# Performance work log

Hardware: AMD Instinct MI355X
Metric: run time of the kernel (lower is better)

## Reference

```python
import jax, jax.numpy as jnp
import numpy as np

B, N, M, H, NH = 128, 4096, 64, 512, 4
IN, OUT = 256, 256
NH2 = 2 * NH  # read/write heads interleaved: even idx = read, odd idx = write
EPS = 1e-8


def setup_inputs() -> dict:
    key = jax.random.key(0)
    ks = jax.random.split(key, 20)
    nrm = lambda k, shape, s=0.05: (jax.random.normal(k, shape, jnp.float32) * s)
    return {
        'in_data': jax.random.normal(ks[0], (B, IN), jnp.float32),
        'memory': jax.random.normal(ks[1], (B, N, M), jnp.float32) * 0.1,
        'h_prev': jax.random.normal(ks[2], (B, H), jnp.float32),
        'c_prev': jax.random.normal(ks[3], (B, H), jnp.float32),
        'prev_reads': jax.random.normal(ks[4], (NH, B, M), jnp.float32),
        'prev_weights': jax.random.uniform(ks[5], (NH2, B, N), jnp.float32),
        # controller LSTMCell (input = in_data ++ prev_reads)
        'W_ih': nrm(ks[6], (4 * H, IN + NH * M)),
        'b_ih': jnp.zeros((4 * H,), jnp.float32),
        'W_hh': nrm(ks[7], (4 * H, H)),
        'b_hh': jnp.zeros((4 * H,), jnp.float32),
        # output layer over [h ++ reads]
        'W_out': nrm(ks[8], (OUT, H + NH * M)),
        'b_out': jnp.zeros((OUT,), jnp.float32),
        # per-head addressing params, stacked over the 2*NH heads (fed with c-state)
        'Wk': nrm(ks[9], (NH2, M, H)), 'bk': jnp.zeros((NH2, M), jnp.float32),
        'Wbeta': nrm(ks[10], (NH2, H)), 'bbeta': jnp.zeros((NH2,), jnp.float32),
        'Wg': nrm(ks[11], (NH2, H)), 'bg': jnp.zeros((NH2,), jnp.float32),
        'Ws': nrm(ks[12], (NH2, 3, H)), 'bs': jnp.zeros((NH2, 3), jnp.float32),
        'Wgam': nrm(ks[13], (NH2, H)), 'bgam': jnp.zeros((NH2,), jnp.float32),
        'We': nrm(ks[14], (NH2, M, H)), 'be': jnp.zeros((NH2, M), jnp.float32),
        'Wa': nrm(ks[15], (NH2, M, H)), 'ba': jnp.zeros((NH2, M), jnp.float32),
    }


def reference(in_data, memory, h_prev, c_prev, prev_reads, prev_weights,
              W_ih, b_ih, W_hh, b_hh, W_out, b_out,
              Wk, bk, Wbeta, bbeta, Wg, bg, Ws, bs, Wgam, bgam, We, be, Wa, ba):
    bsz = in_data.shape[0]
    # controller LSTM step on [x ++ prev_reads]
    x = jnp.concatenate([in_data, jnp.swapaxes(prev_reads, 0, 1).reshape(bsz, -1)], axis=-1)
    gates = x @ W_ih.T + h_prev @ W_hh.T + b_ih + b_hh
    gi, gf, gg, go = jnp.split(gates, 4, axis=-1)
    c = jax.nn.sigmoid(gf) * c_prev + jax.nn.sigmoid(gi) * jnp.tanh(gg)
    h = jax.nn.sigmoid(go) * jnp.tanh(c)  # |h| < 1, so clamp(-20, 20) is identity

    mem = memory
    reads = []
    for i in range(NH2):  # fixed small loop; even = read head, odd = write head
        keyv = c @ Wk[i].T + bk[i]                                    # [B, M]
        beta = jax.nn.softplus(c @ Wbeta[i] + bbeta[i])[:, None]      # [B, 1]
        g = jax.nn.sigmoid(c @ Wg[i] + bg[i])[:, None]                # [B, 1]
        s = jax.nn.softmax(c @ Ws[i].T + bs[i], axis=-1)              # [B, 3]
        gamma = 1.0 + jax.nn.softplus(c @ Wgam[i] + bgam[i])[:, None]  # [B, 1]
        # content addressing: cosine similarity, sharpened softmax
        sim = jnp.einsum('bnm,bm->bn', mem, keyv)
        sim = sim / (jnp.linalg.norm(mem, axis=-1) * jnp.linalg.norm(keyv, axis=-1, keepdims=True) + EPS)
        wc = jax.nn.softmax(beta * sim, axis=-1)
        # interpolate, circular shift (-1, 0, +1), sharpen
        wg_ = g * wc + (1.0 - g) * prev_weights[i]
        wsft = (s[:, 0:1] * jnp.roll(wg_, -1, axis=1)
                + s[:, 1:2] * wg_
                + s[:, 2:3] * jnp.roll(wg_, 1, axis=1))
        wpow = wsft ** gamma
        w = wpow / (jnp.sum(wpow, axis=1, keepdims=True) + EPS)
        if i % 2 == 0:
            reads.append(jnp.einsum('bn,bnm->bm', w, mem))
        else:
            e = jax.nn.sigmoid(c @ We[i].T + be[i])                   # erase [B, M]
            a = jnp.tanh(c @ Wa[i].T + ba[i])                         # add   [B, M]
            mem = mem * (1.0 - w[:, :, None] * e[:, None, :]) + w[:, :, None] * a[:, None, :]

    out = jax.nn.sigmoid(jnp.concatenate([h] + reads, axis=-1) @ W_out.T + b_out)
    return out
```

## Files before the change

### kernel.cpp

```cpp
#include <hip/hip_runtime.h>
#include <math.h>

#define BSZ 128
#define NN_ 4096
#define MM_ 64
#define HH_ 512
#define EPSF 1e-8f

__device__ __forceinline__ float sigmoidf_(float x) { return 1.0f / (1.0f + expf(-x)); }
__device__ __forceinline__ float softplusf_(float x) { return fmaxf(x, 0.0f) + log1pf(expf(-fabsf(x))); }

__global__ void k_build_x(const float* __restrict__ in_data, const float* __restrict__ prev_reads,
                          float* __restrict__ x) {
    int idx = blockIdx.x * blockDim.x + threadIdx.x;
    if (idx >= BSZ * 512) return;
    int b = idx >> 9, j = idx & 511;
    float v;
    if (j < 256) v = in_data[b * 256 + j];
    else {
        int hi = (j - 256) >> 6, m = (j - 256) & 63;
        v = prev_reads[(hi * BSZ + b) * 64 + m];
    }
    x[idx] = v;
}

__global__ __launch_bounds__(256) void k_gemm_atk(const float* __restrict__ A,
                                                  const float* __restrict__ W,
                                                  float* __restrict__ C, int Ncols, int K) {
    __shared__ float Alds[64 * 129];
    __shared__ float Wlds[64 * 65];
    int t = threadIdx.x;
    int k0 = blockIdx.y * 64;
    int n0 = blockIdx.x * 64;
    for (int i = 0; i < 8; ++i) {
        int f = t + 256 * i;
        int row = f >> 4, kk = (f & 15) * 4;
        float4 v = *(const float4*)(A + (size_t)row * K + k0 + kk);
        Alds[(kk + 0) * 129 + row] = v.x;
        Alds[(kk + 1) * 129 + row] = v.y;
        Alds[(kk + 2) * 129 + row] = v.z;
        Alds[(kk + 3) * 129 + row] = v.w;
    }
    for (int i = 0; i < 4; ++i) {
        int f = t + 256 * i;
        int o = f >> 4, kk = (f & 15) * 4;
        float4 v = *(const float4*)(W + (size_t)(n0 + o) * K + k0 + kk);
        Wlds[(kk + 0) * 65 + o] = v.x;
        Wlds[(kk + 1) * 65 + o] = v.y;
        Wlds[(kk + 2) * 65 + o] = v.z;
        Wlds[(kk + 3) * 65 + o] = v.w;
    }
    __syncthreads();
    int ob = (t & 15) * 4;
    int bb = (t >> 4) * 8;
    float acc[4][8];
#pragma unroll
    for (int i = 0; i < 4; ++i)
#pragma unroll
        for (int j = 0; j < 8; ++j) acc[i][j] = 0.f;
    for (int kk = 0; kk < 64; ++kk) {
        const float* wp = &Wlds[kk * 65 + ob];
        const float* ap = &Alds[kk * 129 + bb];
        float w0 = wp[0], w1 = wp[1], w2 = wp[2], w3 = wp[3];
#pragma unroll
        for (int j = 0; j < 8; ++j) {
            float av = ap[j];
            acc[0][j] = fmaf(w0, av, acc[0][j]);
            acc[1][j] = fmaf(w1, av, acc[1][j]);
            acc[2][j] = fmaf(w2, av, acc[2][j]);
            acc[3][j] = fmaf(w3, av, acc[3][j]);
        }
    }
#pragma unroll
    for (int i = 0; i < 4; ++i)
#pragma unroll
        for (int j = 0; j < 8; ++j)
            atomicAdd(&C[(size_t)(bb + j) * Ncols + n0 + ob + i], acc[i][j]);
}

__global__ void k_lstm(const float* __restrict__ gates, const float* __restrict__ b_ih,
                       const float* __restrict__ b_hh, const float* __restrict__ c_prev,
                       float* __restrict__ cbuf, float* __restrict__ hbuf) {
    int idx = blockIdx.x * blockDim.x + threadIdx.x;
    if (idx >= BSZ * HH_) return;
    int b = idx >> 9, j = idx & 511;
    const float* gr = gates + (size_t)b * 2048;
    float gi = gr[j]        + b_ih[j]        + b_hh[j];
    float gf = gr[512 + j]  + b_ih[512 + j]  + b_hh[512 + j];
    float gg = gr[1024 + j] + b_ih[1024 + j] + b_hh[1024 + j];
    float go = gr[1536 + j] + b_ih[1536 + j] + b_hh[1536 + j];
    float cc = sigmoidf_(gf) * c_prev[idx] + sigmoidf_(gi) * tanhf(gg);
    float hh = sigmoidf_(go) * tanhf(cc);
    cbuf[idx] = cc;
    hbuf[idx] = hh;
}

__global__ void k_build_whead(const float* __restrict__ Wk, const float* __restrict__ bk,
                              const float* __restrict__ Wbeta, const float* __restrict__ bbeta,
                              const float* __restrict__ Wg, const float* __restrict__ bg,
                              const float* __restrict__ Ws, const float* __restrict__ bs,
                              const float* __restrict__ Wgam, const float* __restrict__ bgam,
                              const float* __restrict__ We, const float* __restrict__ be,
                              const float* __restrict__ Wa, const float* __restrict__ ba,
                              float* __restrict__ Whead, float* __restrict__ bhead) {
    int idx = blockIdx.x * blockDim.x + threadIdx.x;
    if (idx >= 1600 * 512) return;
    int r = idx >> 9, k = idx & 511;
    float v = 0.f, bv = 0.f;
    if (r < 1584) {
        int i = r / 198, q = r - i * 198;
        if (q < 64)       { v = Wk[((i << 6) + q) * 512 + k];        bv = bk[(i << 6) + q]; }
        else if (q == 64) { v = Wbeta[i * 512 + k];                  bv = bbeta[i]; }
        else if (q == 65) { v = Wg[i * 512 + k];                     bv = bg[i]; }
        else if (q <= 68) { v = Ws[(i * 3 + q - 66) * 512 + k];      bv = bs[i * 3 + q - 66]; }
        else if (q == 69) { v = Wgam[i * 512 + k];                   bv = bgam[i]; }
        else if (q < 134) { v = We[((i << 6) + q - 70) * 512 + k];   bv = be[(i << 6) + q - 70]; }
        else              { v = Wa[((i << 6) + q - 134) * 512 + k];  bv = ba[(i << 6) + q - 134]; }
    }
    Whead[idx] = v;
    if (k == 0) bhead[r] = bv;
}

__global__ __launch_bounds__(256) void k_headact(const float* __restrict__ Chead, const float* __restrict__ bhead,
                                                 float* __restrict__ keys, float* __restrict__ knorm,
                                                 float* __restrict__ betaA, float* __restrict__ gA,
                                                 float* __restrict__ gammaA, float* __restrict__ sA,
                                                 float* __restrict__ eA, float* __restrict__ aA) {
    __shared__ float sk[64];
    __shared__ float s3[3];
    int blk = blockIdx.x;
    int i = blk >> 7, b = blk & 127;
    int q = threadIdx.x;
    float val = 0.f;
    if (q < 198) val = Chead[(size_t)b * 1600 + i * 198 + q] + bhead[i * 198 + q];
    if (q < 64) { keys[(size_t)(i * BSZ + b) * 64 + q] = val; sk[q] = val * val; }
    if (q >= 66 && q <= 68) s3[q - 66] = val;
    __syncthreads();
    if (q == 0) {
        float s = 0.f;
        for (int m2 = 0; m2 < 64; ++m2) s += sk[m2];
        knorm[i * BSZ + b] = sqrtf(s);
    }
    if (q == 64) betaA[i * BSZ + b] = softplusf_(val);
    if (q == 65) gA[i * BSZ + b] = sigmoidf_(val);
    if (q == 69) gammaA[i * BSZ + b] = 1.f + softplusf_(val);
    if (q == 66) {
        float mx = fmaxf(s3[0], fmaxf(s3[1], s3[2]));
        float e0 = expf(s3[0] - mx), e1 = expf(s3[1] - mx), e2 = expf(s3[2] - mx);
        float inv = 1.f / (e0 + e1 + e2);
        sA[(i * BSZ + b) * 3 + 0] = e0 * inv;
        sA[(i * BSZ + b) * 3 + 1] = e1 * inv;
        sA[(i * BSZ + b) * 3 + 2] = e2 * inv;
    }
    if (q >= 70 && q < 134)  eA[(size_t)(i * BSZ + b) * 64 + (q - 70)] = sigmoidf_(val);
    if (q >= 134 && q < 198) aA[(size_t)(i * BSZ + b) * 64 + (q - 134)] = tanhf(val);
}

__global__ __launch_bounds__(256) void k_pass(float* __restrict__ mem,
                                              const float* __restrict__ w_read,
                                              const float* __restrict__ w_write,
                                              const float* __restrict__ e_w, const float* __restrict__ a_w,
                                              const float* __restrict__ k0, const float* __restrict__ k1,
                                              const float* __restrict__ kn0, const float* __restrict__ kn1,
                                              float* __restrict__ sim0, float* __restrict__ sim1,
                                              float* __restrict__ r_out,
                                              int has_read, int has_write, int nsims) {
    __shared__ __align__(16) float rbuf[16][64];
    int t = threadIdx.x;
    int lane = t & 15, grp = t >> 4;
    int base = blockIdx.x * 64;
    int b = base >> 12;
    int m4 = lane * 4;
    float4 e4 = make_float4(0.f, 0.f, 0.f, 0.f), a4 = e4, k0v = e4, k1v = e4;
    float kn0v = 0.f, kn1v = 0.f;
    if (has_write) {
        e4 = *(const float4*)(e_w + b * 64 + m4);
        a4 = *(const float4*)(a_w + b * 64 + m4);
    }
    if (nsims > 0) { k0v = *(const float4*)(k0 + b * 64 + m4); kn0v = kn0[b]; }
    if (nsims > 1) { k1v = *(const float4*)(k1 + b * 64 + m4); kn1v = kn1[b]; }
    float4 racc = make_float4(0.f, 0.f, 0.f, 0.f);
    for (int it = 0; it < 4; ++it) {
        int row = base + it * 16 + grp;
        float4 v = *(const float4*)(mem + (size_t)row * 64 + m4);
        if (has_read) {
            float wr = w_read[row];
            racc.x = fmaf(wr, v.x, racc.x);
            racc.y = fmaf(wr, v.y, racc.y);
            racc.z = fmaf(wr, v.z, racc.z);
            racc.w = fmaf(wr, v.w, racc.w);
        }
        if (has_write) {
            float ww = w_write[row];
            v.x = v.x * (1.f - ww * e4.x) + ww * a4.x;
            v.y = v.y * (1.f - ww * e4.y) + ww * a4.y;
            v.z = v.z * (1.f - ww * e4.z) + ww * a4.z;
            v.w = v.w * (1.f - ww * e4.w) + ww * a4.w;
            *(float4*)(mem + (size_t)row * 64 + m4) = v;
        }
        if (nsims > 0) {
            float d0 = v.x * k0v.x + v.y * k0v.y + v.z * k0v.z + v.w * k0v.w;
            float nn = v.x * v.x + v.y * v.y + v.z * v.z + v.w * v.w;
            float d1 = 0.f;
            if (nsims > 1) d1 = v.x * k1v.x + v.y * k1v.y + v.z * k1v.z + v.w * k1v.w;
#pragma unroll
            for (int off = 8; off >= 1; off >>= 1) {
                d0 += __shfl_xor(d0, off, 16);
                nn += __shfl_xor(nn, off, 16);
                if (nsims > 1) d1 += __shfl_xor(d1, off, 16);
            }
            if (lane == 0) {
                float nm = sqrtf(nn);
                sim0[row] = d0 / (nm * kn0v + EPSF);
                if (nsims > 1) sim1[row] = d1 / (nm * kn1v + EPSF);
            }
        }
    }
    if (has_read) {
        *(float4*)(&rbuf[grp][m4]) = racc;
        __syncthreads();
        if (t < 64) {
            float s = 0.f;
#pragma unroll
            for (int g2 = 0; g2 < 16; ++g2) s += rbuf[g2][t];
            atomicAdd(&r_out[b * 64 + t], s);
        }
    }
}

__global__ __launch_bounds__(256) void k_weights(const float* __restrict__ sims,
                                                 const float* __restrict__ prev_w,
                                                 const float* __restrict__ betaA, const float* __restrict__ gA,
                                                 const float* __restrict__ gammaA, const float* __restrict__ sA,
                                                 float* __restrict__ wout_base, int head0) {
    __shared__ float wg[NN_];
    __shared__ float red[256];
    int h = head0 + blockIdx.y, b = blockIdx.x;
    int hb = h * BSZ + b;
    float beta = betaA[hb], g = gA[hb], gamma = gammaA[hb];
    float s0 = sA[hb * 3 + 0], s1 = sA[hb * 3 + 1], s2 = sA[hb * 3 + 2];
    const float* sim = sims + (size_t)hb * NN_;
    const float* pw = prev_w + (size_t)hb * NN_;
    float* wout = wout_base + (size_t)hb * NN_;
    int t = threadIdx.x;
    float tv[16];
    float lmax = -3.4e38f;
#pragma unroll
    for (int j = 0; j < 16; ++j) {
        float x = beta * sim[t + 256 * j];
        tv[j] = x;
        lmax = fmaxf(lmax, x);
    }
    red[t] = lmax; __syncthreads();
    for (int s = 128; s > 0; s >>= 1) { if (t < s) red[t] = fmaxf(red[t], red[t + s]); __syncthreads(); }
    float Mx = red[0]; __syncthreads();
    float lsum = 0.f;
#pragma unroll
    for (int j = 0; j < 16; ++j) { float ex = expf(tv[j] - Mx); tv[j] = ex; lsum += ex; }
    red[t] = lsum; __syncthreads();
    for (int s = 128; s > 0; s >>= 1) { if (t < s) red[t] += red[t + s]; __syncthreads(); }
    float invS = 1.f / red[0]; __syncthreads();
#pragma unroll
    for (int j = 0; j < 16; ++j) {
        int n = t + 256 * j;
        wg[n] = g * tv[j] * invS + (1.f - g) * pw[n];
    }
    __syncthreads();
    float lsum2 = 0.f;
#pragma unroll
    for (int j = 0; j < 16; ++j) {
        int n = t + 256 * j;
        float wsft = s0 * wg[(n + 1) & (NN_ - 1)] + s1 * wg[n] + s2 * wg[(n - 1) & (NN_ - 1)];
        float wp = powf(wsft, gamma);
        tv[j] = wp;
        lsum2 += wp;
    }
    red[t] = lsum2; __syncthreads();
    for (int s = 128; s > 0; s >>= 1) { if (t < s) red[t] += red[t + s]; __syncthreads(); }
    float inv2 = 1.f / (red[0] + EPSF);
#pragma unroll
    for (int j = 0; j < 16; ++j) wout[t + 256 * j] = tv[j] * inv2;
}

__global__ void k_build_cat(const float* __restrict__ hbuf, const float* __restrict__ rbuf,
                            float* __restrict__ cat) {
    int idx = blockIdx.x * blockDim.x + threadIdx.x;
    if (idx >= BSZ * 768) return;
    int b = idx / 768, j = idx - b * 768;
    float v;
    if (j < 512) v = hbuf[b * 512 + j];
    else {
        int ri = (j - 512) >> 6, m = (j - 512) & 63;
        v = rbuf[(ri * BSZ + b) * 64 + m];
    }
    cat[idx] = v;
}

__global__ void k_out(const float* __restrict__ outacc, const float* __restrict__ b_out,
                      float* __restrict__ out) {
    int idx = blockIdx.x * blockDim.x + threadIdx.x;
    if (idx >= BSZ * 256) return;
    out[idx] = sigmoidf_(outacc[idx] + b_out[idx & 255]);
}

extern "C" void kernel_launch(void* const* d_in, const int* in_sizes, int n_in,
                              void* d_out, int out_size, void* d_ws, size_t ws_size,
                              hipStream_t stream) {
    const float* in_data      = (const float*)d_in[0];
    float*       memory       = (float*)d_in[1];
    const float* h_prev       = (const float*)d_in[2];
    const float* c_prev       = (const float*)d_in[3];
    const float* prev_reads   = (const float*)d_in[4];
    const float* prev_weights = (const float*)d_in[5];
    const float* W_ih = (const float*)d_in[6];
    const float* b_ih = (const float*)d_in[7];
    const float* W_hh = (const float*)d_in[8];
    const float* b_hh = (const float*)d_in[9];
    const float* W_out = (const float*)d_in[10];
    const float* b_out = (const float*)d_in[11];
    const float* Wk   = (const float*)d_in[12];
    const float* bk   = (const float*)d_in[13];
    const float* Wbeta = (const float*)d_in[14];
    const float* bbeta = (const float*)d_in[15];
    const float* Wg   = (const float*)d_in[16];
    const float* bg   = (const float*)d_in[17];
    const float* Ws   = (const float*)d_in[18];
    const float* bs   = (const float*)d_in[19];
    const float* Wgam = (const float*)d_in[20];
    const float* bgam = (const float*)d_in[21];
    const float* We   = (const float*)d_in[22];
    const float* be   = (const float*)d_in[23];
    const float* Wa   = (const float*)d_in[24];
    const float* ba   = (const float*)d_in[25];

    float* ws = (float*)d_ws;
    size_t o_gates  = 0;
    size_t o_chead  = o_gates + 262144;
    size_t o_r      = o_chead + 204800;
    size_t o_outacc = o_r + 32768;
    size_t zero_floats = o_outacc + 32768;
    size_t o_x     = zero_floats;
    size_t o_c     = o_x + 65536;
    size_t o_h     = o_c + 65536;
    size_t o_whead = o_h + 65536;
    size_t o_bhead = o_whead + 819200;
    size_t o_keys  = o_bhead + 2048;
    size_t o_knorm = o_keys + 65536;
    size_t o_beta  = o_knorm + 1024;
    size_t o_g     = o_beta + 1024;
    size_t o_gamma = o_g + 1024;
    size_t o_s     = o_gamma + 1024;
    size_t o_e     = o_s + 3072;
    size_t o_a     = o_e + 65536;
    size_t o_sims  = o_a + 65536;
    size_t o_w     = o_sims + 4194304;
    size_t o_cat   = o_w + 4194304;

    float* gates  = ws + o_gates;
    float* Chead  = ws + o_chead;
    float* rbuf   = ws + o_r;
    float* outacc = ws + o_outacc;
    float* xbuf   = ws + o_x;
    float* cbuf   = ws + o_c;
    float* hbuf   = ws + o_h;
    float* Whead  = ws + o_whead;
    float* bhead  = ws + o_bhead;
    float* keys   = ws + o_keys;
    float* knorm  = ws + o_knorm;
    float* betaA  = ws + o_beta;
    float* gA     = ws + o_g;
    float* gammaA = ws + o_gamma;
    float* sA     = ws + o_s;
    float* eA     = ws + o_e;
    float* aA     = ws + o_a;
    float* sims   = ws + o_sims;
    float* wbuf   = ws + o_w;
    float* cat    = ws + o_cat;

    hipMemsetAsync(d_ws, 0, zero_floats * sizeof(float), stream);

    k_build_x<<<256, 256, 0, stream>>>(in_data, prev_reads, xbuf);
    k_gemm_atk<<<dim3(32, 8), 256, 0, stream>>>(xbuf, W_ih, gates, 2048, 512);
    k_gemm_atk<<<dim3(32, 8), 256, 0, stream>>>(h_prev, W_hh, gates, 2048, 512);
    k_lstm<<<256, 256, 0, stream>>>(gates, b_ih, b_hh, c_prev, cbuf, hbuf);

    k_build_whead<<<3200, 256, 0, stream>>>(Wk, bk, Wbeta, bbeta, Wg, bg, Ws, bs,
                                            Wgam, bgam, We, be, Wa, ba, Whead, bhead);
    k_gemm_atk<<<dim3(25, 8), 256, 0, stream>>>(cbuf, Whead, Chead, 1600, 512);
    k_headact<<<1024, 256, 0, stream>>>(Chead, bhead, keys, knorm, betaA, gA, gammaA, sA, eA, aA);

    const int PB = BSZ * NN_ / 64;
    k_pass<<<PB, 256, 0, stream>>>(memory, nullptr, nullptr, nullptr, nullptr,
                                   keys + 0 * 8192, keys + 1 * 8192, knorm + 0, knorm + 128,
                                   sims + (size_t)0 * 524288, sims + (size_t)1 * 524288,
                                   nullptr, 0, 0, 2);
    k_weights<<<dim3(128, 2), 256, 0, stream>>>(sims, prev_weights, betaA, gA, gammaA, sA, wbuf, 0);
    k_pass<<<PB, 256, 0, stream>>>(memory, wbuf + (size_t)0 * 524288, wbuf + (size_t)1 * 524288,
                                   eA + 1 * 8192, aA + 1 * 8192,
                                   keys + 2 * 8192, keys + 3 * 8192, knorm + 256, knorm + 384,
                                   sims + (size_t)2 * 524288, sims + (size_t)3 * 524288,
                                   rbuf + 0 * 8192, 1, 1, 2);
    k_weights<<<dim3(128, 2), 256, 0, stream>>>(sims, prev_weights, betaA, gA, gammaA, sA, wbuf, 2);
    k_pass<<<PB, 256, 0, stream>>>(memory, wbuf + (size_t)2 * 524288, wbuf + (size_t)3 * 524288,
                                   eA + 3 * 8192, aA + 3 * 8192,
                                   keys + 4 * 8192, keys + 5 * 8192, knorm + 512, knorm + 640,
                                   sims + (size_t)4 * 524288, sims + (size_t)5 * 524288,
                                   rbuf + 1 * 8192, 1, 1, 2);
    k_weights<<<dim3(128, 2), 256, 0, stream>>>(sims, prev_weights, betaA, gA, gammaA, sA, wbuf, 4);
    k_pass<<<PB, 256, 0, stream>>>(memory, wbuf + (size_t)4 * 524288, wbuf + (size_t)5 * 524288,
                                   eA + 5 * 8192, aA + 5 * 8192,
                                   keys + 6 * 8192, nullptr, knorm + 768, nullptr,
                                   sims + (size_t)6 * 524288, nullptr,
                                   rbuf + 2 * 8192, 1, 1, 1);
    k_weights<<<dim3(128, 1), 256, 0, stream>>>(sims, prev_weights, betaA, gA, gammaA, sA, wbuf, 6);
    k_pass<<<PB, 256, 0, stream>>>(memory, wbuf + (size_t)6 * 524288, nullptr,
                                   nullptr, nullptr, nullptr, nullptr, nullptr, nullptr,
                                   nullptr, nullptr, rbuf + 3 * 8192, 1, 0, 0);

    k_build_cat<<<384, 256, 0, stream>>>(hbuf, rbuf, cat);
    k_gemm_atk<<<dim3(4, 12), 256, 0, stream>>>(cat, W_out, outacc, 256, 768);
    k_out<<<128, 256, 0, stream>>>(outacc, b_out, (float*)d_out);

    (void)in_sizes; (void)n_in; (void)out_size; (void)ws_size;
}
```

Before: 573.8 us.

## Recompute memory writes on the fly instead of writing back memory each pass

The memory tensor is no longer modified in place. Each pass reloads the original memory and reapplies the pending erase/add updates from earlier write heads in registers, using the stored write weights, before computing reads and similarities. This removes the per-pass memory store traffic and stops the kernel from mutating its input buffer. In exchange, each later pass reads up to three extra weight vectors and does more arithmetic per element.

```diff
diff --git a/kernel.cpp b/kernel.cpp
--- a/kernel.cpp
+++ b/kernel.cpp
@@ -156,53 +156,77 @@
     if (q >= 134 && q < 198) aA[(size_t)(i * BSZ + b) * 64 + (q - 134)] = tanhf(val);
 }
 
-__global__ __launch_bounds__(256) void k_pass(float* __restrict__ mem,
-                                              const float* __restrict__ w_read,
-                                              const float* __restrict__ w_write,
-                                              const float* __restrict__ e_w, const float* __restrict__ a_w,
-                                              const float* __restrict__ k0, const float* __restrict__ k1,
-                                              const float* __restrict__ kn0, const float* __restrict__ kn1,
-                                              float* __restrict__ sim0, float* __restrict__ sim1,
-                                              float* __restrict__ r_out,
-                                              int has_read, int has_write, int nsims) {
+__global__ __launch_bounds__(256) void k_pass2(const float* __restrict__ mem,
+                                               const float* __restrict__ wbuf,
+                                               const float* __restrict__ eA, const float* __restrict__ aA,
+                                               const float* __restrict__ keys, const float* __restrict__ knorm,
+                                               float* __restrict__ sims, float* __restrict__ r_out,
+                                               int napply, int nsims, int sh0, int sh1,
+                                               int read_state, int read_head, int read_idx) {
     __shared__ __align__(16) float rbuf[16][64];
     int t = threadIdx.x;
     int lane = t & 15, grp = t >> 4;
     int base = blockIdx.x * 64;
     int b = base >> 12;
     int m4 = lane * 4;
-    float4 e4 = make_float4(0.f, 0.f, 0.f, 0.f), a4 = e4, k0v = e4, k1v = e4;
+    float4 e1 = *(const float4*)(eA + (size_t)(1 * BSZ + b) * 64 + m4);
+    float4 a1 = *(const float4*)(aA + (size_t)(1 * BSZ + b) * 64 + m4);
+    float4 e3 = *(const float4*)(eA + (size_t)(3 * BSZ + b) * 64 + m4);
+    float4 a3 = *(const float4*)(aA + (size_t)(3 * BSZ + b) * 64 + m4);
+    float4 e5 = *(const float4*)(eA + (size_t)(5 * BSZ + b) * 64 + m4);
+    float4 a5 = *(const float4*)(aA + (size_t)(5 * BSZ + b) * 64 + m4);
+    float4 k0v = make_float4(0.f, 0.f, 0.f, 0.f), k1v = k0v;
     float kn0v = 0.f, kn1v = 0.f;
-    if (has_write) {
-        e4 = *(const float4*)(e_w + b * 64 + m4);
-        a4 = *(const float4*)(a_w + b * 64 + m4);
-    }
-    if (nsims > 0) { k0v = *(const float4*)(k0 + b * 64 + m4); kn0v = kn0[b]; }
-    if (nsims > 1) { k1v = *(const float4*)(k1 + b * 64 + m4); kn1v = kn1[b]; }
+    if (nsims > 0) { k0v = *(const float4*)(keys + (size_t)(sh0 * BSZ + b) * 64 + m4); kn0v = knorm[sh0 * BSZ + b]; }
+    if (nsims > 1) { k1v = *(const float4*)(keys + (size_t)(sh1 * BSZ + b) * 64 + m4); kn1v = knorm[sh1 * BSZ + b]; }
+    const float* w1p = wbuf + (size_t)1 * BSZ * NN_;
+    const float* w3p = wbuf + (size_t)3 * BSZ * NN_;
+    const float* w5p = wbuf + (size_t)5 * BSZ * NN_;
+    const float* wrp = (read_head >= 0) ? (wbuf + (size_t)read_head * BSZ * NN_) : nullptr;
+    float* sim0 = sims + (size_t)sh0 * BSZ * NN_;
+    float* sim1 = sims + (size_t)sh1 * BSZ * NN_;
+
     float4 racc = make_float4(0.f, 0.f, 0.f, 0.f);
     for (int it = 0; it < 4; ++it) {
         int row = base + it * 16 + grp;
-        float4 v = *(const float4*)(mem + (size_t)row * 64 + m4);
-        if (has_read) {
-            float wr = w_read[row];
-            racc.x = fmaf(wr, v.x, racc.x);
-            racc.y = fmaf(wr, v.y, racc.y);
-            racc.z = fmaf(wr, v.z, racc.z);
-            racc.w = fmaf(wr, v.w, racc.w);
-        }
-        if (has_write) {
-            float ww = w_write[row];
-            v.x = v.x * (1.f - ww * e4.x) + ww * a4.x;
-            v.y = v.y * (1.f - ww * e4.y) + ww * a4.y;
-            v.z = v.z * (1.f - ww * e4.z) + ww * a4.z;
-            v.w = v.w * (1.f - ww * e4.w) + ww * a4.w;
-            *(float4*)(mem + (size_t)row * 64 + m4) = v;
+        float4 m = *(const float4*)(mem + (size_t)row * 64 + m4);
+        float4 mr = m;
+        if (napply >= 1) {
+            float w = w1p[row];
+            m.x = m.x * (1.f - w * e1.x) + w * a1.x;
+            m.y = m.y * (1.f - w * e1.y) + w * a1.y;
+            m.z = m.z * (1.f - w * e1.z) + w * a1.z;
+            m.w = m.w * (1.f - w * e1.w) + w * a1.w;
+            if (read_state == 1) mr = m;
+        }
+        if (napply >= 2) {
+            float w = w3p[row];
+            m.x = m.x * (1.f - w * e3.x) + w * a3.x;
+            m.y = m.y * (1.f - w * e3.y) + w * a3.y;
+            m.z = m.z * (1.f - w * e3.z) + w * a3.z;
+            m.w = m.w * (1.f - w * e3.w) + w * a3.w;
+            if (read_state == 2) mr = m;
+        }
+        if (napply >= 3) {
+            float w = w5p[row];
+            m.x = m.x * (1.f - w * e5.x) + w * a5.x;
+            m.y = m.y * (1.f - w * e5.y) + w * a5.y;
+            m.z = m.z * (1.f - w * e5.z) + w * a5.z;
+            m.w = m.w * (1.f - w * e5.w) + w * a5.w;
+            if (read_state == 3) mr = m;
+        }
+        if (read_head >= 0) {
+            float wr = wrp[row];
+            racc.x = fmaf(wr, mr.x, racc.x);
+            racc.y = fmaf(wr, mr.y, racc.y);
+            racc.z = fmaf(wr, mr.z, racc.z);
+            racc.w = fmaf(wr, mr.w, racc.w);
         }
         if (nsims > 0) {
-            float d0 = v.x * k0v.x + v.y * k0v.y + v.z * k0v.z + v.w * k0v.w;
-            float nn = v.x * v.x + v.y * v.y + v.z * v.z + v.w * v.w;
+            float d0 = m.x * k0v.x + m.y * k0v.y + m.z * k0v.z + m.w * k0v.w;
+            float nn = m.x * m.x + m.y * m.y + m.z * m.z + m.w * m.w;
             float d1 = 0.f;
-            if (nsims > 1) d1 = v.x * k1v.x + v.y * k1v.y + v.z * k1v.z + v.w * k1v.w;
+            if (nsims > 1) d1 = m.x * k1v.x + m.y * k1v.y + m.z * k1v.z + m.w * k1v.w;
 #pragma unroll
             for (int off = 8; off >= 1; off >>= 1) {
                 d0 += __shfl_xor(d0, off, 16);
@@ -216,14 +240,14 @@
             }
         }
     }
-    if (has_read) {
+    if (read_head >= 0) {
         *(float4*)(&rbuf[grp][m4]) = racc;
         __syncthreads();
         if (t < 64) {
             float s = 0.f;
 #pragma unroll
             for (int g2 = 0; g2 < 16; ++g2) s += rbuf[g2][t];
-            atomicAdd(&r_out[b * 64 + t], s);
+            atomicAdd(&r_out[(size_t)(read_idx * BSZ + b) * 64 + t], s);
         }
     }
 }
@@ -307,7 +331,7 @@
                               void* d_out, int out_size, void* d_ws, size_t ws_size,
                               hipStream_t stream) {
     const float* in_data      = (const float*)d_in[0];
-    float*       memory       = (float*)d_in[1];
+    const float* memory       = (const float*)d_in[1];
     const float* h_prev       = (const float*)d_in[2];
     const float* c_prev       = (const float*)d_in[3];
     const float* prev_reads   = (const float*)d_in[4];
@@ -390,32 +414,20 @@
     k_headact<<<1024, 256, 0, stream>>>(Chead, bhead, keys, knorm, betaA, gA, gammaA, sA, eA, aA);
 
     const int PB = BSZ * NN_ / 64;
-    k_pass<<<PB, 256, 0, stream>>>(memory, nullptr, nullptr, nullptr, nullptr,
-                                   keys + 0 * 8192, keys + 1 * 8192, knorm + 0, knorm + 128,
-                                   sims + (size_t)0 * 524288, sims + (size_t)1 * 524288,
-                                   nullptr, 0, 0, 2);
+    k_pass2<<<PB, 256, 0, stream>>>(memory, wbuf, eA, aA, keys, knorm, sims, rbuf,
+                                    0, 2, 0, 1, -1, -1, 0);
     k_weights<<<dim3(128, 2), 256, 0, stream>>>(sims, prev_weights, betaA, gA, gammaA, sA, wbuf, 0);
-    k_pass<<<PB, 256, 0, stream>>>(memory, wbuf + (size_t)0 * 524288, wbuf + (size_t)1 * 524288,
-                                   eA + 1 * 8192, aA + 1 * 8192,
-                                   keys + 2 * 8192, keys + 3 * 8192, knorm + 256, knorm + 384,
-                                   sims + (size_t)2 * 524288, sims + (size_t)3 * 524288,
-                                   rbuf + 0 * 8192, 1, 1, 2);
+    k_pass2<<<PB, 256, 0, stream>>>(memory, wbuf, eA, aA, keys, knorm, sims, rbuf,
+                                    1, 2, 2, 3, 0, 0, 0);
     k_weights<<<dim3(128, 2), 256, 0, stream>>>(sims, prev_weights, betaA, gA, gammaA, sA, wbuf, 2);
-    k_pass<<<PB, 256, 0, stream>>>(memory, wbuf + (size_t)2 * 524288, wbuf + (size_t)3 * 524288,
-                                   eA + 3 * 8192, aA + 3 * 8192,
-                                   keys + 4 * 8192, keys + 5 * 8192, knorm + 512, knorm + 640,
-                                   sims + (size_t)4 * 524288, sims + (size_t)5 * 524288,
-                                   rbuf + 1 * 8192, 1, 1, 2);
+    k_pass2<<<PB, 256, 0, stream>>>(memory, wbuf, eA, aA, keys, knorm, sims, rbuf,
+                                    2, 2, 4, 5, 1, 2, 1);
     k_weights<<<dim3(128, 2), 256, 0, stream>>>(sims, prev_weights, betaA, gA, gammaA, sA, wbuf, 4);
-    k_pass<<<PB, 256, 0, stream>>>(memory, wbuf + (size_t)4 * 524288, wbuf + (size_t)5 * 524288,
-                                   eA + 5 * 8192, aA + 5 * 8192,
-                                   keys + 6 * 8192, nullptr, knorm + 768, nullptr,
-                                   sims + (size_t)6 * 524288, nullptr,
-                                   rbuf + 2 * 8192, 1, 1, 1);
+    k_pass2<<<PB, 256, 0, stream>>>(memory, wbuf, eA, aA, keys, knorm, sims, rbuf,
+                                    3, 1, 6, 6, 2, 4, 2);
     k_weights<<<dim3(128, 1), 256, 0, stream>>>(sims, prev_weights, betaA, gA, gammaA, sA, wbuf, 6);
-    k_pass<<<PB, 256, 0, stream>>>(memory, wbuf + (size_t)6 * 524288, nullptr,
-                                   nullptr, nullptr, nullptr, nullptr, nullptr, nullptr,
-                                   nullptr, nullptr, rbuf + 3 * 8192, 1, 0, 0);
+    k_pass2<<<PB, 256, 0, stream>>>(memory, wbuf, eA, aA, keys, knorm, sims, rbuf,
+                                    3, 0, 0, 0, 3, 6, 3);
 
     k_build_cat<<<384, 256, 0, stream>>>(hbuf, rbuf, cat);
     k_gemm_atk<<<dim3(4, 12), 256, 0, stream>>>(cat, W_out, outacc, 256, 768);
```

Result: faster. 556.6 us (-3.0%).
